# Optimization experiments

Measured on AMD Instinct MI355X. Metric: run time of the kernel, lower is better.

Reference implementation:

```python
import jax, jax.numpy as jnp
import numpy as np

TEMP_LP = 0.05  # args.temp_lp_loss


def setup_inputs() -> dict:
    key = jax.random.key(0)
    k1, k2, k3, k4 = jax.random.split(key, 4)
    B, B_s, topk, C, n_ids = 4096, 4096, 4, 128, 751
    feats = jax.random.normal(k1, (B, C), dtype=jnp.float32)
    feats_s = jax.random.normal(k2, (B_s, topk, C), dtype=jnp.float32)
    labels = jax.random.randint(k3, (B,), 0, n_ids)
    labels_s = jax.random.randint(k4, (B_s * topk,), 0, n_ids)
    return {"feats": feats, "feats_s": feats_s, "labels": labels, "labels_s": labels_s}


def reference(feats, feats_s, labels, labels_s):
    # feats: [B, C]; feats_s: [B_s, topk, C] -> [N, C] with N = B_s*topk
    B, C = feats.shape
    fs = feats_s.reshape(-1, C)
    sim = (feats @ fs.T) / TEMP_LP                      # [B, N]
    # Per-sample: target puts weight 1/P on the P positives (labels_s == label),
    # 0 on negatives. Concatenation order does not affect log_softmax values, so
    # loss_i = -(1/P) * sum_{j in pos} (sim[i,j] - logsumexp(sim[i,:]))
    lse = jax.nn.logsumexpsim = None
    lse = jax.nn.logsumexp(sim, axis=1)                 # [B]
    pos = labels[:, None] == labels_s[None, :]          # [B, N] bool
    P = pos.sum(axis=1).astype(sim.dtype)               # [B]
    pos_sum = jnp.sum(jnp.where(pos, sim, jnp.zeros((), sim.dtype)), axis=1)
    loss_i = lse - pos_sum / P                          # [B]
    return jnp.sum(loss_i) / B
```

## Files before the change

### kernel.cpp

```cpp
#include <hip/hip_runtime.h>
#include <hip/hip_bf16.h>

#define B_ROWS 4096
#define N_COLS 16384
#define CDIM   128
#define NIDS   751
#define TEMP_INV 20.0f
#define ASCALE 28.853900817779268f
#define LN2 0.6931471805599453f
#define THR 32.0f

#define NCHUNK 32
#define CPC (N_COLS / NCHUNK)
#define TSTEPS (CPC / 16)
#define LSE_BLOCKS 512
#define POS_BLOCKS (N_COLS / 256)
#define NLBL NIDS

typedef __attribute__((ext_vector_type(8))) short short8;
typedef __attribute__((ext_vector_type(4))) float f32x4;
typedef __attribute__((ext_vector_type(4))) unsigned short u16x4;

__device__ __forceinline__ unsigned short f2bf(float x) {
  union { float f; unsigned u; } c; c.f = x;
  unsigned r = c.u + 0x7FFFu + ((c.u >> 16) & 1u);
  return (unsigned short)(r >> 16);
}

__global__ void prep_kernel(const float* __restrict__ feats, const float* __restrict__ fs,
                            const int* __restrict__ labels, const int* __restrict__ labels_s,
                            unsigned short* __restrict__ feats_bf, unsigned short* __restrict__ fs_bf,
                            float* __restrict__ Ftab, float* __restrict__ Pcnt,
                            float* __restrict__ acc) {
  const int bid = blockIdx.x;
  const int tid = threadIdx.x;
  if (bid < NLBL) {
    __shared__ int list[64];
    __shared__ int cnt;
    __shared__ float red[4];
    if (tid == 0) cnt = 0;
    if (bid == 0 && tid < 4) acc[tid] = 0.f;
    __syncthreads();
    const int4* lab4 = (const int4*)labels;
#pragma unroll
    for (int it = 0; it < 4; ++it) {
      int idx = it * 256 + tid;
      int4 v = lab4[idx];
      int r0 = idx * 4;
      if (v.x == bid) { int k = atomicAdd(&cnt, 1); if (k < 64) list[k] = r0; }
      if (v.y == bid) { int k = atomicAdd(&cnt, 1); if (k < 64) list[k] = r0 + 1; }
      if (v.z == bid) { int k = atomicAdd(&cnt, 1); if (k < 64) list[k] = r0 + 2; }
      if (v.w == bid) { int k = atomicAdd(&cnt, 1); if (k < 64) list[k] = r0 + 3; }
    }
    const int4* ls4 = (const int4*)labels_s;
    int c = 0;
#pragma unroll 4
    for (int it = 0; it < 16; ++it) {
      int4 v = ls4[it * 256 + tid];
      c += (v.x == bid) + (v.y == bid) + (v.z == bid) + (v.w == bid);
    }
#pragma unroll
    for (int off = 1; off < 64; off <<= 1) c += __shfl_xor(c, off, 64);
    if ((tid & 63) == 0) red[tid >> 6] = (float)c;
    __syncthreads();
    int n = min(cnt, 64);
    if (tid < CDIM) {
      float a = 0.f;
      for (int k = 0; k < n; ++k) a += feats[(size_t)list[k] * CDIM + tid];
      Ftab[(size_t)bid * CDIM + tid] = a;
    } else if (tid == CDIM) {
      Pcnt[bid] = red[0] + red[1] + red[2] + red[3];
    }
  } else {
    const int NF4 = B_ROWS * CDIM / 4;
    int idx = (bid - NLBL) * 256 + tid;
    if (idx < NF4) {
      f32x4 v = ((const f32x4*)feats)[idx];
      u16x4 o = { f2bf(v[0] * ASCALE), f2bf(v[1] * ASCALE), f2bf(v[2] * ASCALE), f2bf(v[3] * ASCALE) };
      ((u16x4*)feats_bf)[idx] = o;
    } else {
      int j = idx - NF4;
      f32x4 v = ((const f32x4*)fs)[j];
      u16x4 o = { f2bf(v[0]), f2bf(v[1]), f2bf(v[2]), f2bf(v[3]) };
      ((u16x4*)fs_bf)[j] = o;
    }
  }
}

__launch_bounds__(256, 2)
__global__ void main_kernel(const unsigned short* __restrict__ A,
                            const unsigned short* __restrict__ Bm,
                            const float* __restrict__ fs32,
                            const int* __restrict__ labels_s,
                            const float* __restrict__ Ftab, const float* __restrict__ Pcnt,
                            float* __restrict__ pmL,
                            float* __restrict__ acc) {
  const int tid = threadIdx.x;

  if (blockIdx.x < POS_BLOCKS) {
    __shared__ float wsum[4];
    int j = blockIdx.x * 256 + tid;
    int l = labels_s[j];
    const f32x4* fr = (const f32x4*)(fs32 + (size_t)j * CDIM);
    const f32x4* Fr = (const f32x4*)(Ftab + (size_t)l * CDIM);
    float d = 0.f;
#pragma unroll
    for (int q = 0; q < CDIM / 4; ++q) {
      f32x4 a = fr[q], b = Fr[q];
      d += a[0] * b[0] + a[1] * b[1] + a[2] * b[2] + a[3] * b[3];
    }
    d /= Pcnt[l];
#pragma unroll
    for (int off = 1; off < 64; off <<= 1) d += __shfl_xor(d, off, 64);
    if ((tid & 63) == 0) wsum[tid >> 6] = d;
    __syncthreads();
    if (tid == 0) atomicAdd(&acc[1], wsum[0] + wsum[1] + wsum[2] + wsum[3]);
    return;
  }

  const int lseb = blockIdx.x - POS_BLOCKS;
  const int wv = tid >> 6, ln = tid & 63;
  const int hi = ln >> 4, lo = ln & 15;
  const int ch = lseb & (NCHUNK - 1);
  const int rowg = ((lseb >> 5) << 2) | wv;
  const int row0 = rowg * 64;

  const unsigned short* aptr = A + (size_t)(row0 + lo) * CDIM + hi * 8;
  short8 afr[4][4];
#pragma unroll
  for (int rg = 0; rg < 4; ++rg)
#pragma unroll
    for (int kk = 0; kk < 4; ++kk)
      afr[rg][kk] = *(const short8*)(aptr + rg * 16 * CDIM + kk * 32);

  float m_[16], s_[16];
#pragma unroll
  for (int g = 0; g < 16; ++g) { m_[g] = -1e30f; s_[g] = 0.f; }

  const unsigned short* bptr = Bm + (size_t)(ch * CPC + lo) * CDIM + hi * 8;
  short8 bcur[4], bnxt[4];
#pragma unroll
  for (int kk = 0; kk < 4; ++kk) bcur[kk] = *(const short8*)(bptr + kk * 32);
  bptr += 16 * CDIM;

  for (int t = 0; t < TSTEPS; ++t) {
    if (t + 1 < TSTEPS) {
#pragma unroll
      for (int kk = 0; kk < 4; ++kk) bnxt[kk] = *(const short8*)(bptr + kk * 32);
      bptr += 16 * CDIM;
    }

    f32x4 av[4];
#pragma unroll
    for (int rg = 0; rg < 4; ++rg) {
      f32x4 c4 = {0.f, 0.f, 0.f, 0.f};
#pragma unroll
      for (int kk = 0; kk < 4; ++kk)
        c4 = __builtin_amdgcn_mfma_f32_16x16x32_bf16(afr[rg][kk], bcur[kk], c4, 0, 0, 0);
      av[rg] = c4;
    }

    float d_[16], dm = -1e30f;
#pragma unroll
    for (int rg = 0; rg < 4; ++rg)
#pragma unroll
      for (int j = 0; j < 4; ++j) {
        d_[rg * 4 + j] = av[rg][j] - m_[rg * 4 + j];
        dm = fmaxf(dm, d_[rg * 4 + j]);
      }
    if (__any(dm > THR)) {
#pragma unroll
      for (int rg = 0; rg < 4; ++rg)
#pragma unroll
        for (int j = 0; j < 4; ++j) {
          int g = rg * 4 + j;
          float v = av[rg][j];
          float mn = fmaxf(m_[g], v);
          s_[g] = s_[g] * __builtin_amdgcn_exp2f(m_[g] - mn)
                + __builtin_amdgcn_exp2f(v - mn);
          m_[g] = mn;
        }
    } else {
#pragma unroll
      for (int g = 0; g < 16; ++g) s_[g] += __builtin_amdgcn_exp2f(d_[g]);
    }

#pragma unroll
    for (int kk = 0; kk < 4; ++kk) bcur[kk] = bnxt[kk];
  }

#pragma unroll
  for (int off = 1; off < 16; off <<= 1) {
#pragma unroll
    for (int g = 0; g < 16; ++g) {
      float mo = __shfl_xor(m_[g], off, 64);
      float so = __shfl_xor(s_[g], off, 64);
      float mn = fmaxf(m_[g], mo);
      s_[g] = s_[g] * __builtin_amdgcn_exp2f(m_[g] - mn)
            + so * __builtin_amdgcn_exp2f(mo - mn);
      m_[g] = mn;
    }
  }

  if (lo == 0) {
#pragma unroll
    for (int g = 0; g < 16; ++g) {
      int row = row0 + (g >> 2) * 16 + hi * 4 + (g & 3);
      pmL[(size_t)ch * B_ROWS + row] = m_[g] + __log2f(s_[g]);
    }
  }
}

__global__ void combine_kernel(const float* __restrict__ pmL,
                               float* __restrict__ acc,
                               float* __restrict__ out) {
  int row = blockIdx.x * blockDim.x + threadIdx.x;
  float L[NCHUNK];
  float mg = -1e30f;
#pragma unroll
  for (int c = 0; c < NCHUNK; ++c) {
    L[c] = pmL[c * B_ROWS + row];
    mg = fmaxf(mg, L[c]);
  }
  float sg = 0.f;
#pragma unroll
  for (int c = 0; c < NCHUNK; ++c) sg += __builtin_amdgcn_exp2f(L[c] - mg);
  float lse = LN2 * mg + logf(sg);
#pragma unroll
  for (int off = 1; off < 64; off <<= 1) lse += __shfl_xor(lse, off, 64);
  __shared__ float wsum[4];
  if ((threadIdx.x & 63) == 0) wsum[threadIdx.x >> 6] = lse;
  __syncthreads();
  if (threadIdx.x == 0) {
    atomicAdd(&acc[0], wsum[0] + wsum[1] + wsum[2] + wsum[3]);
    __threadfence();
    unsigned old = atomicAdd((unsigned*)&acc[2], 1u);
    if (old == (B_ROWS / 256) - 1) {
      float a0 = atomicAdd(&acc[0], 0.f);
      float a1 = atomicAdd(&acc[1], 0.f);
      out[0] = (a0 - TEMP_INV * a1) * (1.0f / (float)B_ROWS);
    }
  }
}

extern "C" void kernel_launch(void* const* d_in, const int* in_sizes, int n_in,
                              void* d_out, int out_size, void* d_ws, size_t ws_size,
                              hipStream_t stream) {
  const float* feats   = (const float*)d_in[0];
  const float* feats_s = (const float*)d_in[1];
  const int* labels    = (const int*)d_in[2];
  const int* labels_s  = (const int*)d_in[3];
  float* out = (float*)d_out;

  char* ws = (char*)d_ws;
  size_t off = 0;
  auto carve = [&](size_t bytes) -> char* {
    char* p = ws + off;
    off += (bytes + 255) & ~(size_t)255;
    return p;
  };
  unsigned short* feats_bf = (unsigned short*)carve((size_t)B_ROWS * CDIM * 2);
  unsigned short* fs_bf    = (unsigned short*)carve((size_t)N_COLS * CDIM * 2);
  float* Ftab = (float*)carve((size_t)NIDS * CDIM * 4);
  float* Pcnt = (float*)carve((size_t)NIDS * 4);
  float* pmL  = (float*)carve((size_t)NCHUNK * B_ROWS * 4);
  float* acc  = (float*)carve(4 * 4);

  const int NCVT = (B_ROWS * CDIM / 4 + N_COLS * CDIM / 4) / 256;
  prep_kernel<<<NLBL + NCVT, 256, 0, stream>>>(feats, feats_s, labels, labels_s,
                                               feats_bf, fs_bf, Ftab, Pcnt, acc);
  main_kernel<<<POS_BLOCKS + LSE_BLOCKS, 256, 0, stream>>>(feats_bf, fs_bf, feats_s, labels_s,
                                                           Ftab, Pcnt, pmL, acc);
  combine_kernel<<<B_ROWS / 256, 256, 0, stream>>>(pmL, acc, out);
}
```

Measured before the change: 122.2 us.

## Shrink per-wave row tile, double chunk count, and ping-pong B loads in LSE kernel

Each wave now covers 32 rows instead of 64, and the column dimension is split into 64 chunks instead of 32. This yields 2048 LSE blocks and lower register pressure, which allows launch bounds of 3 blocks per CU. The inner loop is unrolled by two with alternating B register buffers and uses s_setprio around the MFMA sequence to favour matrix issue. Per-wave A-fragment reuse drops and B data is reloaded twice as often across row groups. The combine kernel reads twice as many partials per row, and the B workspace is padded because the last iteration prefetches one tile past the end.

```diff
diff --git a/kernel.cpp b/kernel.cpp
--- a/kernel.cpp
+++ b/kernel.cpp
@@ -10,10 +10,11 @@
 #define LN2 0.6931471805599453f
 #define THR 32.0f
 
-#define NCHUNK 32
+#define NCHUNK 64
 #define CPC (N_COLS / NCHUNK)
 #define TSTEPS (CPC / 16)
-#define LSE_BLOCKS 512
+#define ROWBLK 128
+#define LSE_BLOCKS ((B_ROWS / ROWBLK) * NCHUNK)
 #define POS_BLOCKS (N_COLS / 256)
 #define NLBL NIDS
 
@@ -87,7 +88,7 @@
   }
 }
 
-__launch_bounds__(256, 2)
+__launch_bounds__(256, 3)
 __global__ void main_kernel(const unsigned short* __restrict__ A,
                             const unsigned short* __restrict__ Bm,
                             const float* __restrict__ fs32,
@@ -122,59 +123,52 @@
   const int wv = tid >> 6, ln = tid & 63;
   const int hi = ln >> 4, lo = ln & 15;
   const int ch = lseb & (NCHUNK - 1);
-  const int rowg = ((lseb >> 5) << 2) | wv;
-  const int row0 = rowg * 64;
+  const int row0 = (lseb >> 6) * ROWBLK + wv * 32;
 
   const unsigned short* aptr = A + (size_t)(row0 + lo) * CDIM + hi * 8;
-  short8 afr[4][4];
-#pragma unroll
-  for (int rg = 0; rg < 4; ++rg)
+  short8 afr[2][4];
+#pragma unroll
+  for (int rg = 0; rg < 2; ++rg)
 #pragma unroll
     for (int kk = 0; kk < 4; ++kk)
       afr[rg][kk] = *(const short8*)(aptr + rg * 16 * CDIM + kk * 32);
 
-  float m_[16], s_[16];
-#pragma unroll
-  for (int g = 0; g < 16; ++g) { m_[g] = -1e30f; s_[g] = 0.f; }
+  float m_[8], s_[8];
+#pragma unroll
+  for (int g = 0; g < 8; ++g) { m_[g] = -1e30f; s_[g] = 0.f; }
 
   const unsigned short* bptr = Bm + (size_t)(ch * CPC + lo) * CDIM + hi * 8;
-  short8 bcur[4], bnxt[4];
-#pragma unroll
-  for (int kk = 0; kk < 4; ++kk) bcur[kk] = *(const short8*)(bptr + kk * 32);
+  short8 bA[4], bB[4];
+#pragma unroll
+  for (int kk = 0; kk < 4; ++kk) bA[kk] = *(const short8*)(bptr + kk * 32);
   bptr += 16 * CDIM;
 
-  for (int t = 0; t < TSTEPS; ++t) {
-    if (t + 1 < TSTEPS) {
-#pragma unroll
-      for (int kk = 0; kk < 4; ++kk) bnxt[kk] = *(const short8*)(bptr + kk * 32);
-      bptr += 16 * CDIM;
-    }
-
-    f32x4 av[4];
-#pragma unroll
-    for (int rg = 0; rg < 4; ++rg) {
+  auto step = [&](const short8* b) {
+    f32x4 av[2];
+    __builtin_amdgcn_s_setprio(1);
+#pragma unroll
+    for (int rg = 0; rg < 2; ++rg) {
       f32x4 c4 = {0.f, 0.f, 0.f, 0.f};
 #pragma unroll
       for (int kk = 0; kk < 4; ++kk)
-        c4 = __builtin_amdgcn_mfma_f32_16x16x32_bf16(afr[rg][kk], bcur[kk], c4, 0, 0, 0);
+        c4 = __builtin_amdgcn_mfma_f32_16x16x32_bf16(afr[rg][kk], b[kk], c4, 0, 0, 0);
       av[rg] = c4;
     }
-
-    float d_[16], dm = -1e30f;
-#pragma unroll
-    for (int rg = 0; rg < 4; ++rg)
-#pragma unroll
-      for (int j = 0; j < 4; ++j) {
-        d_[rg * 4 + j] = av[rg][j] - m_[rg * 4 + j];
-        dm = fmaxf(dm, d_[rg * 4 + j]);
-      }
+    __builtin_amdgcn_s_setprio(0);
+#pragma unroll
+    for (int rg = 0; rg < 2; ++rg)
+#pragma unroll
+      for (int j = 0; j < 4; ++j)
+        av[rg][j] -= m_[rg * 4 + j];
+    float dm = fmaxf(fmaxf(fmaxf(av[0][0], av[0][1]), fmaxf(av[0][2], av[0][3])),
+                     fmaxf(fmaxf(av[1][0], av[1][1]), fmaxf(av[1][2], av[1][3])));
     if (__any(dm > THR)) {
 #pragma unroll
-      for (int rg = 0; rg < 4; ++rg)
+      for (int rg = 0; rg < 2; ++rg)
 #pragma unroll
         for (int j = 0; j < 4; ++j) {
           int g = rg * 4 + j;
-          float v = av[rg][j];
+          float v = av[rg][j] + m_[g];
           float mn = fmaxf(m_[g], v);
           s_[g] = s_[g] * __builtin_amdgcn_exp2f(m_[g] - mn)
                 + __builtin_amdgcn_exp2f(v - mn);
@@ -182,17 +176,29 @@
         }
     } else {
 #pragma unroll
-      for (int g = 0; g < 16; ++g) s_[g] += __builtin_amdgcn_exp2f(d_[g]);
-    }
-
-#pragma unroll
-    for (int kk = 0; kk < 4; ++kk) bcur[kk] = bnxt[kk];
+      for (int rg = 0; rg < 2; ++rg)
+#pragma unroll
+        for (int j = 0; j < 4; ++j)
+          s_[rg * 4 + j] += __builtin_amdgcn_exp2f(av[rg][j]);
+    }
+  };
+
+#pragma unroll 1
+  for (int t = 0; t < TSTEPS; t += 2) {
+#pragma unroll
+    for (int kk = 0; kk < 4; ++kk) bB[kk] = *(const short8*)(bptr + kk * 32);
+    bptr += 16 * CDIM;
+    step(bA);
+#pragma unroll
+    for (int kk = 0; kk < 4; ++kk) bA[kk] = *(const short8*)(bptr + kk * 32);
+    bptr += 16 * CDIM;
+    step(bB);
   }
 
 #pragma unroll
   for (int off = 1; off < 16; off <<= 1) {
 #pragma unroll
-    for (int g = 0; g < 16; ++g) {
+    for (int g = 0; g < 8; ++g) {
       float mo = __shfl_xor(m_[g], off, 64);
       float so = __shfl_xor(s_[g], off, 64);
       float mn = fmaxf(m_[g], mo);
@@ -204,7 +210,7 @@
 
   if (lo == 0) {
 #pragma unroll
-    for (int g = 0; g < 16; ++g) {
+    for (int g = 0; g < 8; ++g) {
       int row = row0 + (g >> 2) * 16 + hi * 4 + (g & 3);
       pmL[(size_t)ch * B_ROWS + row] = m_[g] + __log2f(s_[g]);
     }
@@ -215,16 +221,13 @@
                                float* __restrict__ acc,
                                float* __restrict__ out) {
   int row = blockIdx.x * blockDim.x + threadIdx.x;
-  float L[NCHUNK];
   float mg = -1e30f;
 #pragma unroll
-  for (int c = 0; c < NCHUNK; ++c) {
-    L[c] = pmL[c * B_ROWS + row];
-    mg = fmaxf(mg, L[c]);
-  }
+  for (int c = 0; c < NCHUNK; ++c) mg = fmaxf(mg, pmL[c * B_ROWS + row]);
   float sg = 0.f;
 #pragma unroll
-  for (int c = 0; c < NCHUNK; ++c) sg += __builtin_amdgcn_exp2f(L[c] - mg);
+  for (int c = 0; c < NCHUNK; ++c)
+    sg += __builtin_amdgcn_exp2f(pmL[c * B_ROWS + row] - mg);
   float lse = LN2 * mg + logf(sg);
 #pragma unroll
   for (int off = 1; off < 64; off <<= 1) lse += __shfl_xor(lse, off, 64);
@@ -260,7 +263,7 @@
     return p;
   };
   unsigned short* feats_bf = (unsigned short*)carve((size_t)B_ROWS * CDIM * 2);
-  unsigned short* fs_bf    = (unsigned short*)carve((size_t)N_COLS * CDIM * 2);
+  unsigned short* fs_bf    = (unsigned short*)carve((size_t)(N_COLS + 16) * CDIM * 2);
   float* Ftab = (float*)carve((size_t)NIDS * CDIM * 4);
   float* Pcnt = (float*)carve((size_t)NIDS * 4);
   float* pmL  = (float*)carve((size_t)NCHUNK * B_ROWS * 4);
```

Measured after the change: 163.0 us. +33.4%, slower.
